# Kernel tuning notes

Hardware: AMD Instinct MI355X
Metric: run time of the kernel (lower is better)

Reference implementation:

```python
import jax, jax.numpy as jnp
import numpy as np
import math

D_MODEL, D_FF, N_EXPERTS, TOP_K, N_SHARED = 1024, 4096, 8, 2, 1
B, T = 4, 1024
SCALE = 1.0 / math.sqrt(N_SHARED + TOP_K / N_EXPERTS)


def setup_inputs() -> dict:
    key = jax.random.key(0)
    ks = jax.random.split(key, 10)
    s1 = 1.0 / math.sqrt(D_MODEL)
    s2 = 1.0 / math.sqrt(D_FF)
    return {
        "x": jax.random.normal(ks[0], (B, T, D_MODEL), dtype=jnp.float32),
        "w_router": jax.random.normal(ks[1], (N_EXPERTS, D_MODEL), dtype=jnp.float32) * s1,
        "W1": jax.random.normal(ks[2], (N_EXPERTS, D_FF, D_MODEL), dtype=jnp.float32) * s1,
        "b1": jax.random.normal(ks[3], (N_EXPERTS, D_FF), dtype=jnp.float32) * 0.02,
        "W2": jax.random.normal(ks[4], (N_EXPERTS, D_MODEL, D_FF), dtype=jnp.float32) * s2,
        "b2": jax.random.normal(ks[5], (N_EXPERTS, D_MODEL), dtype=jnp.float32) * 0.02,
        "Ws1": jax.random.normal(ks[6], (D_FF, D_MODEL), dtype=jnp.float32) * s1,
        "bs1": jax.random.normal(ks[7], (D_FF,), dtype=jnp.float32) * 0.02,
        "Ws2": jax.random.normal(ks[8], (D_MODEL, D_FF), dtype=jnp.float32) * s2,
        "bs2": jax.random.normal(ks[9], (D_MODEL,), dtype=jnp.float32) * 0.02,
    }


def reference(x, w_router, W1, b1, W2, b2, Ws1, bs1, Ws2, bs2):
    # Router: logits -> softmax -> top-k gate values (no renormalization, matching source)
    logits = jnp.einsum("btd,ed->bte", x, w_router)      # [B,T,E]
    probs = jax.nn.softmax(logits, axis=-1)
    vals, idx = jax.lax.top_k(probs, TOP_K)               # [B,T,K]
    # Scatter top-k gate values into dense per-expert gates [B,T,E]
    gates = jnp.sum(jax.nn.one_hot(idx, N_EXPERTS, dtype=x.dtype) * vals[..., None], axis=-2)

    # Shared (always-on) expert FFN
    hs = jax.nn.gelu(jnp.einsum("btd,fd->btf", x, Ws1) + bs1)
    acc = jnp.einsum("btf,df->btd", hs, Ws2) + bs2

    # Routed experts, densified combine: sum_e gate[b,t,e] * FFN_e(x[b,t])
    h = jax.nn.gelu(jnp.einsum("btd,efd->btef", x, W1) + b1)   # [B,T,E,F]
    y = jnp.einsum("btef,edf->bted", h, W2) + b2               # [B,T,E,D]
    acc = acc + jnp.einsum("bted,bte->btd", y, gates)

    return SCALE * acc
```

## Files before the change

### kernel.cpp

```cpp
#include <hip/hip_runtime.h>
#include <hip/hip_bf16.h>

#define NTOK 4096
#define DM   1024
#define DF   4096
#define ROWS_TOTAL 12288
#define BM 128
#define BN 128
#define BK 64
#define SCALE_F 0.8944271909999159f
#define PMAX 103

typedef __attribute__((ext_vector_type(8))) short short8;
typedef __attribute__((ext_vector_type(4))) float floatx4;

#define GLD16(gp, lp) __builtin_amdgcn_global_load_lds( \
    (const __attribute__((address_space(1))) void*)(gp), \
    (__attribute__((address_space(3))) void*)(lp), 16, 0, 0)

__device__ __forceinline__ ushort f2bf(float f){
    __hip_bfloat16 h = __float2bfloat16(f);
    return *reinterpret_cast<ushort*>(&h);
}

__device__ __forceinline__ float gelu_tanh(float v){
    float u2 = -1.5957691216057308f * (v + 0.044715f * v * v * v);
    return v / (1.0f + __expf(u2));
}

#define CV8_N0 524288u
#define CV8_N1 4718592u
#define CV8_N2 8912896u
#define CV8_N3 9437184u
#define CV8_N4 9961472u
__global__ __launch_bounds__(256) void cvt_all(
    const float* __restrict__ x,  const float* __restrict__ W1,
    const float* __restrict__ W2, const float* __restrict__ Ws1,
    const float* __restrict__ Ws2,
    ushort* __restrict__ xb,  ushort* __restrict__ w1b, ushort* __restrict__ w2b,
    ushort* __restrict__ ws1b, ushort* __restrict__ ws2b)
{
    unsigned i = blockIdx.x * 256u + threadIdx.x;
    const float* s; ushort* d; unsigned off;
    if      (i < CV8_N0){ s = x;   d = xb;   off = i; }
    else if (i < CV8_N1){ s = W1;  d = w1b;  off = i - CV8_N0; }
    else if (i < CV8_N2){ s = W2;  d = w2b;  off = i - CV8_N1; }
    else if (i < CV8_N3){ s = Ws1; d = ws1b; off = i - CV8_N2; }
    else                { s = Ws2; d = ws2b; off = i - CV8_N3; }
    const float4* s4 = reinterpret_cast<const float4*>(s) + 2 * (size_t)off;
    float4 a = s4[0];
    float4 b = s4[1];
    short8 o;
    o[0] = (short)f2bf(a.x); o[1] = (short)f2bf(a.y);
    o[2] = (short)f2bf(a.z); o[3] = (short)f2bf(a.w);
    o[4] = (short)f2bf(b.x); o[5] = (short)f2bf(b.y);
    o[6] = (short)f2bf(b.z); o[7] = (short)f2bf(b.w);
    reinterpret_cast<short8*>(d)[off] = o;
}

__global__ __launch_bounds__(256) void router_kernel(
    const float* __restrict__ x, const float* __restrict__ wr,
    int* __restrict__ te, float* __restrict__ tg, int* __restrict__ tokarr)
{
    const int token = blockIdx.x * 4 + (threadIdx.x >> 6);
    const int lane  = threadIdx.x & 63;
    const float* xp = x + (size_t)token * DM;
    float s[8];
    #pragma unroll
    for (int e = 0; e < 8; e++) s[e] = 0.f;
    for (int d = lane; d < DM; d += 64){
        float xv = xp[d];
        #pragma unroll
        for (int e = 0; e < 8; e++) s[e] += xv * wr[e * DM + d];
    }
    #pragma unroll
    for (int e = 0; e < 8; e++){
        float v = s[e];
        #pragma unroll
        for (int off = 32; off > 0; off >>= 1) v += __shfl_down(v, off);
        s[e] = v;
    }
    if (lane == 0){
        float m = s[0];
        #pragma unroll
        for (int e = 1; e < 8; e++) m = fmaxf(m, s[e]);
        float p[8]; float sum = 0.f;
        #pragma unroll
        for (int e = 0; e < 8; e++){ p[e] = __expf(s[e] - m); sum += p[e]; }
        float inv = 1.f / sum;
        #pragma unroll
        for (int e = 0; e < 8; e++) p[e] *= inv;
        int i1 = 0; float p1 = p[0];
        #pragma unroll
        for (int e = 1; e < 8; e++) if (p[e] > p1){ p1 = p[e]; i1 = e; }
        int i2 = -1; float p2 = -1.f;
        #pragma unroll
        for (int e = 0; e < 8; e++) if (e != i1 && p[e] > p2){ p2 = p[e]; i2 = e; }
        te[token*2+0] = i1; te[token*2+1] = i2;
        tg[token*2+0] = p1; tg[token*2+1] = p2;
        tokarr[token] = token;
    }
}

__global__ __launch_bounds__(256) void plan_kernel(
    const int* __restrict__ te, int* __restrict__ tokarr,
    int* __restrict__ rowof, int* __restrict__ meta)
{
    __shared__ int lc[9], lcur[9];
    const int t = threadIdx.x;
    if (t < 9) lc[t] = 0;
    __syncthreads();
    for (int j = t; j < NTOK*2; j += 256) atomicAdd(&lc[te[j]], 1);
    __syncthreads();
    if (t == 0){
        int off = NTOK;
        for (int e = 0; e < 8; e++){
            lcur[e]    = off;
            meta[e]    = lc[e];
            meta[16+e] = off;
            meta[32+e] = (lc[e] + BM - 1) / BM;
            off += lc[e];
        }
        meta[8]    = NTOK;
        meta[16+8] = 0;
        meta[32+8] = NTOK / BM;
    }
    __syncthreads();
    for (int j = t; j < NTOK*2; j += 256){
        int e = te[j];
        int p = atomicAdd(&lcur[e], 1);
        tokarr[p] = j >> 1;
        rowof[j]  = p;
    }
}

template<int MODE>
__global__ __launch_bounds__(256) void gemm_kernel(
    const ushort* __restrict__ Abase,
    const ushort* __restrict__ Wb, const ushort* __restrict__ Wsb,
    const float* __restrict__ brout, const float* __restrict__ bsh,
    const int* __restrict__ meta, const int* __restrict__ tokarr,
    ushort* __restrict__ Hout, float* __restrict__ Yout)
{
    const int xcd = blockIdx.x & 7;
    const int q   = blockIdx.x >> 3;
    const int NTG = (MODE == 0) ? 4 : 1;

    int e = -1, r = 0, a0 = 0;
    #pragma unroll
    for (int ee = 0; ee < 9; ee++){
        int w = NTG * meta[32 + ee];
        if (e < 0 && q < a0 + w){ e = ee; r = q - a0; }
        a0 += w;
    }
    if (e < 0) return;
    const int mt_e = meta[32 + e];
    int ntg, mti;
    if (MODE == 0){ ntg = r / mt_e; mti = r - ntg * mt_e; }
    else          { ntg = 0;        mti = r; }
    const int nt   = (MODE == 0) ? (xcd + 8 * ntg) : xcd;
    const int cnt  = meta[e];
    const int base = meta[16 + e];

    const int K = (MODE == 0) ? DM : DF;
    const int N = (MODE == 0) ? DF : DM;
    const ushort* Bp  = (e < 8) ? (Wb + (size_t)e * DF * DM) : Wsb;
    const float* bias = (e < 8) ? (brout + e * N) : bsh;

    __shared__ ushort As[2][BM * BK];
    __shared__ ushort Bs[2][BN * BK];

    const int t    = threadIdx.x;
    const int lane = t & 63;
    const int wv   = t >> 6;
    const int wm   = (wv >> 1) * 64;
    const int wn   = (wv & 1) * 64;
    const int lrow = lane & 15;
    const int quad = lane >> 4;
    const int swz8 = ((lane & 7) ^ (lane >> 3)) * 8;

    const ushort* Ap[4];
    const ushort* Bpp[4];
    ushort* Alds0[4]; ushort* Alds1[4];
    ushort* Blds0[4]; ushort* Blds1[4];
    #pragma unroll
    for (int i = 0; i < 4; i++){
        int rin = wv * 32 + i * 8 + (lane >> 3);
        int pos = mti * BM + rin;
        int clp = (pos < cnt) ? pos : (cnt - 1);
        if (MODE == 0) Ap[i] = Abase + (size_t)tokarr[base + clp] * DM + swz8;
        else           Ap[i] = Abase + (size_t)(base + clp) * DF + swz8;
        Bpp[i]   = Bp + (size_t)(nt * BN + rin) * K + swz8;
        Alds0[i] = &As[0][(wv * 32 + i * 8) * BK];
        Alds1[i] = &As[1][(wv * 32 + i * 8) * BK];
        Blds0[i] = &Bs[0][(wv * 32 + i * 8) * BK];
        Blds1[i] = &Bs[1][(wv * 32 + i * 8) * BK];
    }

    floatx4 acc[4][4];
    #pragma unroll
    for (int mi = 0; mi < 4; mi++)
        #pragma unroll
        for (int ni = 0; ni < 4; ni++)
            acc[mi][ni] = (floatx4){0.f, 0.f, 0.f, 0.f};

    auto phase = [&](const ushort* Asb, const ushort* Bsb,
                     ushort* const* Aldsn, ushort* const* Bldsn,
                     int knext, bool pf){
        short8 af0[4], bf0[4], af1[4], bf1[4];
        #pragma unroll
        for (int mi = 0; mi < 4; mi++){
            int row = wm + mi * 16 + lrow;
            int p0  = (0 + quad) ^ (row & 7);
            int p1  = (4 + quad) ^ (row & 7);
            af0[mi] = *reinterpret_cast<const short8*>(&Asb[row * BK + p0 * 8]);
            af1[mi] = *reinterpret_cast<const short8*>(&Asb[row * BK + p1 * 8]);
        }
        #pragma unroll
        for (int ni = 0; ni < 4; ni++){
            int row = wn + ni * 16 + lrow;
            int p0  = (0 + quad) ^ (row & 7);
            int p1  = (4 + quad) ^ (row & 7);
            bf0[ni] = *reinterpret_cast<const short8*>(&Bsb[row * BK + p0 * 8]);
            bf1[ni] = *reinterpret_cast<const short8*>(&Bsb[row * BK + p1 * 8]);
        }
        __builtin_amdgcn_sched_barrier(0);
        if (pf){
            #pragma unroll
            for (int i = 0; i < 4; i++){
                GLD16(Ap[i]  + knext, Aldsn[i]);
                GLD16(Bpp[i] + knext, Bldsn[i]);
            }
        }
        __builtin_amdgcn_sched_barrier(0);
        #pragma unroll
        for (int mi = 0; mi < 4; mi++)
            #pragma unroll
            for (int ni = 0; ni < 4; ni++)
                acc[mi][ni] = __builtin_amdgcn_mfma_f32_16x16x32_bf16(af0[mi], bf0[ni], acc[mi][ni], 0, 0, 0);
        #pragma unroll
        for (int mi = 0; mi < 4; mi++)
            #pragma unroll
            for (int ni = 0; ni < 4; ni++)
                acc[mi][ni] = __builtin_amdgcn_mfma_f32_16x16x32_bf16(af1[mi], bf1[ni], acc[mi][ni], 0, 0, 0);
        __syncthreads();
    };

    #pragma unroll
    for (int i = 0; i < 4; i++){
        GLD16(Ap[i], Alds0[i]);
        GLD16(Bpp[i], Blds0[i]);
    }
    __syncthreads();

    #pragma unroll 1
    for (int k0 = 0; k0 < K; k0 += 2 * BK){
        phase(As[0], Bs[0], Alds1, Blds1, k0 + BK,     true);
        phase(As[1], Bs[1], Alds0, Blds0, k0 + 2 * BK, k0 + 2 * BK < K);
    }

    float bv[4];
    #pragma unroll
    for (int ni = 0; ni < 4; ni++) bv[ni] = bias[nt * BN + wn + ni*16 + lrow];

    #pragma unroll
    for (int mi = 0; mi < 4; mi++){
        #pragma unroll
        for (int rg = 0; rg < 4; rg++){
            int s   = wm + mi*16 + quad*4 + rg;
            int pos = mti * BM + s;
            if (pos >= cnt) continue;
            int rr = base + pos;
            if (MODE == 0){
                ushort* hp = Hout + (size_t)rr * DF + nt * BN;
                #pragma unroll
                for (int ni = 0; ni < 4; ni++){
                    float v = acc[mi][ni][rg] + bv[ni];
                    hp[wn + ni*16 + lrow] = f2bf(gelu_tanh(v));
                }
            } else {
                float* yp = Yout + (size_t)rr * DM + nt * BN;
                #pragma unroll
                for (int ni = 0; ni < 4; ni++)
                    yp[wn + ni*16 + lrow] = acc[mi][ni][rg] + bv[ni];
            }
        }
    }
}

__global__ __launch_bounds__(256) void combine_kernel(
    const float* __restrict__ Y, const int* __restrict__ rowof,
    const float* __restrict__ tg, float* __restrict__ out)
{
    const int token = blockIdx.x;
    const int d4    = threadIdx.x;
    const float4* Y4 = reinterpret_cast<const float4*>(Y);
    int r1 = rowof[token*2+0], r2 = rowof[token*2+1];
    float g1 = tg[token*2+0],  g2 = tg[token*2+1];
    float4 a = Y4[(size_t)token * 256 + d4];
    float4 b = Y4[(size_t)r1 * 256 + d4];
    float4 c = Y4[(size_t)r2 * 256 + d4];
    float4 o;
    o.x = SCALE_F * (a.x + g1*b.x + g2*c.x);
    o.y = SCALE_F * (a.y + g1*b.y + g2*c.y);
    o.z = SCALE_F * (a.z + g1*b.z + g2*c.z);
    o.w = SCALE_F * (a.w + g1*b.w + g2*c.w);
    reinterpret_cast<float4*>(out)[(size_t)token * 256 + d4] = o;
}

extern "C" void kernel_launch(void* const* d_in, const int* in_sizes, int n_in,
                              void* d_out, int out_size, void* d_ws, size_t ws_size,
                              hipStream_t stream) {
    const float* x   = (const float*)d_in[0];
    const float* wr  = (const float*)d_in[1];
    const float* W1  = (const float*)d_in[2];
    const float* b1  = (const float*)d_in[3];
    const float* W2  = (const float*)d_in[4];
    const float* b2  = (const float*)d_in[5];
    const float* Ws1 = (const float*)d_in[6];
    const float* bs1 = (const float*)d_in[7];
    const float* Ws2 = (const float*)d_in[8];
    const float* bs2 = (const float*)d_in[9];
    float* out = (float*)d_out;

    char* ws = (char*)d_ws;
    size_t off = 0;
    auto wsalloc = [&](size_t bytes) -> char* {
        char* p = ws + off;
        off += (bytes + 255) & ~(size_t)255;
        return p;
    };
    ushort* xb   = (ushort*)wsalloc((size_t)NTOK * DM * 2);
    ushort* w1b  = (ushort*)wsalloc((size_t)8 * DF * DM * 2);
    ushort* w2b  = (ushort*)wsalloc((size_t)8 * DM * DF * 2);
    ushort* ws1b = (ushort*)wsalloc((size_t)DF * DM * 2);
    ushort* ws2b = (ushort*)wsalloc((size_t)DM * DF * 2);
    ushort* H    = (ushort*)wsalloc((size_t)ROWS_TOTAL * DF * 2);
    int*    tokarr = (int*)wsalloc(ROWS_TOTAL * 4);
    int*    rowof  = (int*)wsalloc(NTOK * 2 * 4);
    int*    te     = (int*)wsalloc(NTOK * 2 * 4);
    float*  tg     = (float*)wsalloc(NTOK * 2 * 4);
    int*    meta   = (int*)wsalloc(64 * 4);
    float*  Y = (float*)w1b;

    cvt_all<<<CV8_N4/256, 256, 0, stream>>>(x, W1, W2, Ws1, Ws2,
                                            xb, w1b, w2b, ws1b, ws2b);
    router_kernel<<<NTOK/4, 256, 0, stream>>>(x, wr, te, tg, tokarr);
    plan_kernel<<<1, 256, 0, stream>>>(te, tokarr, rowof, meta);

    gemm_kernel<0><<<8 * 4 * PMAX, 256, 0, stream>>>(xb, w1b, ws1b, b1, bs1,
        meta, tokarr, H, Y);
    gemm_kernel<1><<<8 * PMAX, 256, 0, stream>>>(H, w2b, ws2b, b2, bs2,
        meta, tokarr, H, Y);

    combine_kernel<<<NTOK, 256, 0, stream>>>(Y, rowof, tg, out);
}
```

Before: 731.2 us.

## Fuse fp32-to-bf16 weight conversion into GEMM B-tile loads

Removes the separate pass that converts all expert and shared weights to bf16. The GEMM kernels now read fp32 weights directly into registers, convert them and store swizzled bf16 into LDS, while A tiles still come in through direct global-to-LDS loads. This drops a full read-and-write pass over about 80 MB of weights. In exchange, fp32 weight traffic inside the GEMMs doubles, and since each weight tile is reread by many M-tiles, the conversion work is repeated and register pressure rises. Y also gets its own workspace allocation instead of reusing the old bf16 weight buffer.

Measured after the change: 1.051 ms. 1.44x slower.

```diff
diff --git a/kernel.cpp b/kernel.cpp
--- a/kernel.cpp
+++ b/kernel.cpp
@@ -28,26 +28,11 @@
     return v / (1.0f + __expf(u2));
 }
 
-#define CV8_N0 524288u
-#define CV8_N1 4718592u
-#define CV8_N2 8912896u
-#define CV8_N3 9437184u
-#define CV8_N4 9961472u
-__global__ __launch_bounds__(256) void cvt_all(
-    const float* __restrict__ x,  const float* __restrict__ W1,
-    const float* __restrict__ W2, const float* __restrict__ Ws1,
-    const float* __restrict__ Ws2,
-    ushort* __restrict__ xb,  ushort* __restrict__ w1b, ushort* __restrict__ w2b,
-    ushort* __restrict__ ws1b, ushort* __restrict__ ws2b)
+__global__ __launch_bounds__(256) void cvt_x(
+    const float* __restrict__ x, ushort* __restrict__ xb)
 {
     unsigned i = blockIdx.x * 256u + threadIdx.x;
-    const float* s; ushort* d; unsigned off;
-    if      (i < CV8_N0){ s = x;   d = xb;   off = i; }
-    else if (i < CV8_N1){ s = W1;  d = w1b;  off = i - CV8_N0; }
-    else if (i < CV8_N2){ s = W2;  d = w2b;  off = i - CV8_N1; }
-    else if (i < CV8_N3){ s = Ws1; d = ws1b; off = i - CV8_N2; }
-    else                { s = Ws2; d = ws2b; off = i - CV8_N3; }
-    const float4* s4 = reinterpret_cast<const float4*>(s) + 2 * (size_t)off;
+    const float4* s4 = reinterpret_cast<const float4*>(x) + 2 * (size_t)i;
     float4 a = s4[0];
     float4 b = s4[1];
     short8 o;
@@ -55,7 +40,7 @@
     o[2] = (short)f2bf(a.z); o[3] = (short)f2bf(a.w);
     o[4] = (short)f2bf(b.x); o[5] = (short)f2bf(b.y);
     o[6] = (short)f2bf(b.z); o[7] = (short)f2bf(b.w);
-    reinterpret_cast<short8*>(d)[off] = o;
+    reinterpret_cast<short8*>(xb)[i] = o;
 }
 
 __global__ __launch_bounds__(256) void router_kernel(
@@ -137,7 +122,7 @@
 template<int MODE>
 __global__ __launch_bounds__(256) void gemm_kernel(
     const ushort* __restrict__ Abase,
-    const ushort* __restrict__ Wb, const ushort* __restrict__ Wsb,
+    const float* __restrict__ Wf, const float* __restrict__ Wsf,
     const float* __restrict__ brout, const float* __restrict__ bsh,
     const int* __restrict__ meta, const int* __restrict__ tokarr,
     ushort* __restrict__ Hout, float* __restrict__ Yout)
@@ -164,11 +149,11 @@
 
     const int K = (MODE == 0) ? DM : DF;
     const int N = (MODE == 0) ? DF : DM;
-    const ushort* Bp  = (e < 8) ? (Wb + (size_t)e * DF * DM) : Wsb;
+    const float* Bf   = (e < 8) ? (Wf + (size_t)e * DF * DM) : Wsf;
     const float* bias = (e < 8) ? (brout + e * N) : bsh;
 
-    __shared__ ushort As[2][BM * BK];
-    __shared__ ushort Bs[2][BN * BK];
+    __shared__ __align__(16) ushort As[2][BM * BK];
+    __shared__ __align__(16) ushort Bs[2][BN * BK];
 
     const int t    = threadIdx.x;
     const int lane = t & 63;
@@ -180,9 +165,7 @@
     const int swz8 = ((lane & 7) ^ (lane >> 3)) * 8;
 
     const ushort* Ap[4];
-    const ushort* Bpp[4];
-    ushort* Alds0[4]; ushort* Alds1[4];
-    ushort* Blds0[4]; ushort* Blds1[4];
+    int Aoff[4];
     #pragma unroll
     for (int i = 0; i < 4; i++){
         int rin = wv * 32 + i * 8 + (lane >> 3);
@@ -190,12 +173,16 @@
         int clp = (pos < cnt) ? pos : (cnt - 1);
         if (MODE == 0) Ap[i] = Abase + (size_t)tokarr[base + clp] * DM + swz8;
         else           Ap[i] = Abase + (size_t)(base + clp) * DF + swz8;
-        Bpp[i]   = Bp + (size_t)(nt * BN + rin) * K + swz8;
-        Alds0[i] = &As[0][(wv * 32 + i * 8) * BK];
-        Alds1[i] = &As[1][(wv * 32 + i * 8) * BK];
-        Blds0[i] = &Bs[0][(wv * 32 + i * 8) * BK];
-        Blds1[i] = &Bs[1][(wv * 32 + i * 8) * BK];
-    }
+        Aoff[i] = (wv * 32 + i * 8) * BK;
+    }
+
+    const int rB = t >> 1;
+    const int h  = t & 1;
+    const float* BpF = Bf + (size_t)(nt * BN + rB) * K + h * 32;
+    int wrOff[4];
+    #pragma unroll
+    for (int k = 0; k < 4; k++)
+        wrOff[k] = rB * BK + (((h * 4 + k) ^ (rB & 7)) * 8);
 
     floatx4 acc[4][4];
     #pragma unroll
@@ -204,33 +191,49 @@
         for (int ni = 0; ni < 4; ni++)
             acc[mi][ni] = (floatx4){0.f, 0.f, 0.f, 0.f};
 
-    auto phase = [&](const ushort* Asb, const ushort* Bsb,
-                     ushort* const* Aldsn, ushort* const* Bldsn,
-                     int knext, bool pf){
-        short8 af0[4], bf0[4], af1[4], bf1[4];
+    auto bload = [&](float4* br, int kg){
+        const float4* src = reinterpret_cast<const float4*>(BpF + kg);
+        #pragma unroll
+        for (int j = 0; j < 8; j++) br[j] = src[j];
+    };
+    auto bstore = [&](const float4* br, ushort* BsN){
+        #pragma unroll
+        for (int k = 0; k < 4; k++){
+            float4 u = br[2*k], v = br[2*k+1];
+            short8 o;
+            o[0] = (short)f2bf(u.x); o[1] = (short)f2bf(u.y);
+            o[2] = (short)f2bf(u.z); o[3] = (short)f2bf(u.w);
+            o[4] = (short)f2bf(v.x); o[5] = (short)f2bf(v.y);
+            o[6] = (short)f2bf(v.z); o[7] = (short)f2bf(v.w);
+            *reinterpret_cast<short8*>(&BsN[wrOff[k]]) = o;
+        }
+    };
+
+    auto phase = [&](const ushort* AsC, const ushort* BsC,
+                     ushort* AsN, ushort* BsN, int knext, bool pf){
+        short8 af0[4], af1[4], bf0[4], bf1[4];
         #pragma unroll
         for (int mi = 0; mi < 4; mi++){
             int row = wm + mi * 16 + lrow;
             int p0  = (0 + quad) ^ (row & 7);
             int p1  = (4 + quad) ^ (row & 7);
-            af0[mi] = *reinterpret_cast<const short8*>(&Asb[row * BK + p0 * 8]);
-            af1[mi] = *reinterpret_cast<const short8*>(&Asb[row * BK + p1 * 8]);
+            af0[mi] = *reinterpret_cast<const short8*>(&AsC[row * BK + p0 * 8]);
+            af1[mi] = *reinterpret_cast<const short8*>(&AsC[row * BK + p1 * 8]);
         }
         #pragma unroll
         for (int ni = 0; ni < 4; ni++){
             int row = wn + ni * 16 + lrow;
             int p0  = (0 + quad) ^ (row & 7);
             int p1  = (4 + quad) ^ (row & 7);
-            bf0[ni] = *reinterpret_cast<const short8*>(&Bsb[row * BK + p0 * 8]);
-            bf1[ni] = *reinterpret_cast<const short8*>(&Bsb[row * BK + p1 * 8]);
+            bf0[ni] = *reinterpret_cast<const short8*>(&BsC[row * BK + p0 * 8]);
+            bf1[ni] = *reinterpret_cast<const short8*>(&BsC[row * BK + p1 * 8]);
         }
         __builtin_amdgcn_sched_barrier(0);
+        float4 br[8];
         if (pf){
             #pragma unroll
-            for (int i = 0; i < 4; i++){
-                GLD16(Ap[i]  + knext, Aldsn[i]);
-                GLD16(Bpp[i] + knext, Bldsn[i]);
-            }
+            for (int i = 0; i < 4; i++) GLD16(Ap[i] + knext, AsN + Aoff[i]);
+            bload(br, knext);
         }
         __builtin_amdgcn_sched_barrier(0);
         #pragma unroll
@@ -243,20 +246,23 @@
             #pragma unroll
             for (int ni = 0; ni < 4; ni++)
                 acc[mi][ni] = __builtin_amdgcn_mfma_f32_16x16x32_bf16(af1[mi], bf1[ni], acc[mi][ni], 0, 0, 0);
+        if (pf) bstore(br, BsN);
         __syncthreads();
     };
 
-    #pragma unroll
-    for (int i = 0; i < 4; i++){
-        GLD16(Ap[i], Alds0[i]);
-        GLD16(Bpp[i], Blds0[i]);
-    }
-    __syncthreads();
+    {
+        #pragma unroll
+        for (int i = 0; i < 4; i++) GLD16(Ap[i], &As[0][Aoff[i]]);
+        float4 br[8];
+        bload(br, 0);
+        bstore(br, Bs[0]);
+        __syncthreads();
+    }
 
     #pragma unroll 1
     for (int k0 = 0; k0 < K; k0 += 2 * BK){
-        phase(As[0], Bs[0], Alds1, Blds1, k0 + BK,     true);
-        phase(As[1], Bs[1], Alds0, Blds0, k0 + 2 * BK, k0 + 2 * BK < K);
+        phase(As[0], Bs[0], As[1], Bs[1], k0 + BK,     true);
+        phase(As[1], Bs[1], As[0], Bs[0], k0 + 2 * BK, k0 + 2 * BK < K);
     }
 
     float bv[4];
@@ -331,26 +337,21 @@
         return p;
     };
     ushort* xb   = (ushort*)wsalloc((size_t)NTOK * DM * 2);
-    ushort* w1b  = (ushort*)wsalloc((size_t)8 * DF * DM * 2);
-    ushort* w2b  = (ushort*)wsalloc((size_t)8 * DM * DF * 2);
-    ushort* ws1b = (ushort*)wsalloc((size_t)DF * DM * 2);
-    ushort* ws2b = (ushort*)wsalloc((size_t)DM * DF * 2);
     ushort* H    = (ushort*)wsalloc((size_t)ROWS_TOTAL * DF * 2);
+    float*  Y    = (float*) wsalloc((size_t)ROWS_TOTAL * DM * 4);
     int*    tokarr = (int*)wsalloc(ROWS_TOTAL * 4);
     int*    rowof  = (int*)wsalloc(NTOK * 2 * 4);
     int*    te     = (int*)wsalloc(NTOK * 2 * 4);
     float*  tg     = (float*)wsalloc(NTOK * 2 * 4);
     int*    meta   = (int*)wsalloc(64 * 4);
-    float*  Y = (float*)w1b;
-
-    cvt_all<<<CV8_N4/256, 256, 0, stream>>>(x, W1, W2, Ws1, Ws2,
-                                            xb, w1b, w2b, ws1b, ws2b);
+
+    cvt_x<<<2048, 256, 0, stream>>>(x, xb);
     router_kernel<<<NTOK/4, 256, 0, stream>>>(x, wr, te, tg, tokarr);
     plan_kernel<<<1, 256, 0, stream>>>(te, tokarr, rowof, meta);
 
-    gemm_kernel<0><<<8 * 4 * PMAX, 256, 0, stream>>>(xb, w1b, ws1b, b1, bs1,
+    gemm_kernel<0><<<8 * 4 * PMAX, 256, 0, stream>>>(xb, W1, Ws1, b1, bs1,
         meta, tokarr, H, Y);
-    gemm_kernel<1><<<8 * PMAX, 256, 0, stream>>>(H, w2b, ws2b, b2, bs2,
+    gemm_kernel<1><<<8 * PMAX, 256, 0, stream>>>(H, W2, Ws2, b2, bs2,
         meta, tokarr, H, Y);
 
     combine_kernel<<<NTOK, 256, 0, stream>>>(Y, rowof, tg, out);
```
